# Optimization experiments

Hardware: AMD Instinct MI355X
Metric: run time of the kernel (lower is better)

## Reference

```python
import jax, jax.numpy as jnp
import numpy as np

HID = 1024
HEADS = 16
HEAD_DIM = HID // HEADS
MLP_HID = 4096
TEMB = 1024
EPS = 1e-6


def _ln(x):
    # LayerNorm without affine, eps=1e-6
    mu = jnp.mean(x, axis=-1, keepdims=True)
    var = jnp.var(x, axis=-1, keepdims=True)
    return (x - mu) * jax.lax.rsqrt(var + EPS)


def _modulate(x, shift, scale):
    return x * (1.0 + scale[:, None, :]) + shift[:, None, :]


def setup_inputs() -> dict:
    key = jax.random.key(0)
    ks = jax.random.split(key, 12)
    s = 0.02
    return {
        "x": jax.random.normal(ks[0], (8, 1024, HID), jnp.float32),
        "c": jax.random.normal(ks[1], (8, TEMB), jnp.float32),
        "W_qkv": jax.random.normal(ks[2], (HID, 3 * HID), jnp.float32) * s,
        "b_qkv": jnp.zeros((3 * HID,), jnp.float32),
        "W_proj": jax.random.normal(ks[3], (HID, HID), jnp.float32) * s,
        "b_proj": jnp.zeros((HID,), jnp.float32),
        "W_fc1": jax.random.normal(ks[4], (HID, MLP_HID), jnp.float32) * s,
        "b_fc1": jnp.zeros((MLP_HID,), jnp.float32),
        "W_fc2": jax.random.normal(ks[5], (MLP_HID, HID), jnp.float32) * s,
        "b_fc2": jnp.zeros((HID,), jnp.float32),
        "W_ada": jax.random.normal(ks[6], (TEMB, 6 * HID), jnp.float32) * s,
        "b_ada": jnp.zeros((6 * HID,), jnp.float32),
    }


def _attn(x, W_qkv, b_qkv, W_proj, b_proj):
    B, N, C = x.shape
    qkv = x @ W_qkv + b_qkv                      # [B,N,3C]
    qkv = qkv.reshape(B, N, 3, HEADS, HEAD_DIM)
    q, k, v = qkv[:, :, 0], qkv[:, :, 1], qkv[:, :, 2]  # [B,N,H,D]
    scale = HEAD_DIM ** -0.5
    logits = jnp.einsum('bnhd,bmhd->bhnm', q, k) * scale
    attn = jax.nn.softmax(logits, axis=-1)
    out = jnp.einsum('bhnm,bmhd->bnhd', attn, v).reshape(B, N, C)
    return out @ W_proj + b_proj


def reference(x, c, W_qkv, b_qkv, W_proj, b_proj, W_fc1, b_fc1, W_fc2, b_fc2, W_ada, b_ada):
    ada = jax.nn.silu(c) @ W_ada + b_ada          # [B,6C]
    shift_msa, scale_msa, gate_msa, shift_mlp, scale_mlp, gate_mlp = jnp.split(ada, 6, axis=1)

    h = _modulate(_ln(x), shift_msa, scale_msa)
    x = x + gate_msa[:, None, :] * _attn(h, W_qkv, b_qkv, W_proj, b_proj)

    h = _modulate(_ln(x), shift_mlp, scale_mlp)
    h = jax.nn.gelu(h @ W_fc1 + b_fc1, approximate=True) @ W_fc2 + b_fc2
    x = x + gate_mlp[:, None, :] * h
    return x
```

## Files before the change

### kernel.cpp

```cpp
#include <hip/hip_runtime.h>
#include <stdint.h>

typedef unsigned short u16;
typedef __attribute__((ext_vector_type(4))) float f32x4;
typedef __attribute__((ext_vector_type(8))) short bf16x8;
typedef bf16x8 bf16x8a __attribute__((may_alias));
typedef uint32_t u32a __attribute__((may_alias));

#define HID 1024
#define MLPD 4096
#define TEMB 1024
#define ADA_N 6144
#define SEQ 1024
#define BATCH 8
#define KCH 32
#define KCHLEN (TEMB / KCH)

__device__ __forceinline__ u16 f2bf_bits(float f) {
  uint32_t u = __float_as_uint(f);
  uint32_t r = (u + 0x7FFFu + ((u >> 16) & 1u)) >> 16;
  return (u16)r;
}

__device__ __forceinline__ uint32_t cvt_pk_bf16(float lo, float hi) {
  uint32_t r;
  asm("v_cvt_pk_bf16_f32 %0, %1, %2" : "=v"(r) : "v"(lo), "v"(hi));
  return r;
}

__device__ __forceinline__ float exp2_hw(float x) {
#if __has_builtin(__builtin_amdgcn_exp2f)
  return __builtin_amdgcn_exp2f(x);
#else
  return exp2f(x);
#endif
}

__device__ __forceinline__ void async_copy16(void* lds_dst, const void* g_src) {
  __builtin_amdgcn_global_load_lds(
      (const __attribute__((address_space(1))) void*)(uintptr_t)g_src,
      (__attribute__((address_space(3))) void*)(uint32_t)(uintptr_t)lds_dst,
      16, 0, 0);
}

__device__ __forceinline__ float gelu_tanh(float v) {
  float u = 0.7978845608028654f * (v + 0.044715f * v * v * v);
  float e = __expf(2.f * u);
  return v * e / (e + 1.f);
}

__global__ __launch_bounds__(256) void transpose_bf16(const float* __restrict__ W,
                                                      u16* __restrict__ Wt, int K, int N) {
  __shared__ float tile[32][33];
  int n0 = blockIdx.x * 32, k0 = blockIdx.y * 32;
  int tx = threadIdx.x & 31, ty = threadIdx.x >> 5;
#pragma unroll
  for (int i = 0; i < 4; i++)
    tile[ty + i * 8][tx] = W[(size_t)(k0 + ty + i * 8) * N + n0 + tx];
  __syncthreads();
#pragma unroll
  for (int i = 0; i < 4; i++)
    Wt[(size_t)(n0 + ty + i * 8) * K + k0 + tx] = f2bf_bits(tile[tx][ty + i * 8]);
}

__global__ __launch_bounds__(256) void ada_part(const float* __restrict__ c,
                                                const float* __restrict__ W,
                                                float* __restrict__ part) {
  __shared__ float sc[BATCH * KCHLEN];
  int t = threadIdx.x;
  int col = blockIdx.x * 256 + t;
  int kc = blockIdx.y;
  int k0 = kc * KCHLEN;
  for (int i = t; i < BATCH * KCHLEN; i += 256) {
    int b = i >> 5, kk = i & (KCHLEN - 1);
    float v = c[b * TEMB + k0 + kk];
    sc[i] = v / (1.f + __expf(-v));
  }
  __syncthreads();
  float acc[BATCH] = {};
  for (int kk = 0; kk < KCHLEN; kk++) {
    float w = W[(size_t)(k0 + kk) * ADA_N + col];
#pragma unroll
    for (int b = 0; b < BATCH; b++) acc[b] += sc[b * KCHLEN + kk] * w;
  }
#pragma unroll
  for (int b = 0; b < BATCH; b++)
    part[((size_t)kc * BATCH + b) * ADA_N + col] = acc[b];
}

__global__ __launch_bounds__(256) void ada_reduce(const float* __restrict__ part,
                                                  const float* __restrict__ bias,
                                                  float* __restrict__ out) {
  int i = blockIdx.x * 256 + threadIdx.x;
  int col = i % ADA_N, b = i / ADA_N;
  float s = bias[col];
#pragma unroll
  for (int kc = 0; kc < KCH; kc++)
    s += part[((size_t)kc * BATCH + b) * ADA_N + col];
  out[(size_t)b * ADA_N + col] = s;
}

__global__ __launch_bounds__(256) void ln_mod(const float* __restrict__ x,
                                              const float* __restrict__ ada,
                                              int shift_off, int scale_off,
                                              u16* __restrict__ h) {
  int row = blockIdx.x;
  int bb = row >> 10;
  int t = threadIdx.x;
  const float4 v = ((const float4*)(x + (size_t)row * HID))[t];
  float s = v.x + v.y + v.z + v.w;
  float sq = v.x * v.x + v.y * v.y + v.z * v.z + v.w * v.w;
#pragma unroll
  for (int off = 32; off >= 1; off >>= 1) {
    s += __shfl_xor(s, off);
    sq += __shfl_xor(sq, off);
  }
  __shared__ float red[8];
  int wid = t >> 6;
  if ((t & 63) == 0) { red[wid] = s; red[4 + wid] = sq; }
  __syncthreads();
  s = red[0] + red[1] + red[2] + red[3];
  sq = red[4] + red[5] + red[6] + red[7];
  float mu = s * (1.0f / HID);
  float rs = rsqrtf(sq * (1.0f / HID) - mu * mu + 1e-6f);
  const float4 sc = ((const float4*)(ada + (size_t)bb * ADA_N + scale_off))[t];
  const float4 sh = ((const float4*)(ada + (size_t)bb * ADA_N + shift_off))[t];
  ushort4 o;
  o.x = f2bf_bits((v.x - mu) * rs * (1.f + sc.x) + sh.x);
  o.y = f2bf_bits((v.y - mu) * rs * (1.f + sc.y) + sh.y);
  o.z = f2bf_bits((v.z - mu) * rs * (1.f + sc.z) + sh.z);
  o.w = f2bf_bits((v.w - mu) * rs * (1.f + sc.w) + sh.w);
  ((ushort4*)(h + (size_t)row * HID))[t] = o;
}


template <int NLOAD>
__device__ __forceinline__ void stage_tile(u16* dst, const u16* gsrc, int K, int koff, int t) {
#pragma unroll
  for (int i = 0; i < NLOAD; ++i) {
    int slot = i * 512 + t;
    int row = slot >> 3, cp = slot & 7;
    const u16* src = gsrc + (size_t)row * K + koff + ((cp ^ (row & 7)) << 3);
    async_copy16(dst + slot * 8, src);
  }
}

#define LDSRD(buf, row, kk) \
  (*(const bf16x8a*)&(buf)[(row) * 64 + ((((kk) * 4 + l4) ^ ((row) & 7)) << 3)])

template <int EPI, int BN>
__global__ __launch_bounds__(512, 2) void gemm8(const u16* __restrict__ A,
                                                const u16* __restrict__ Bt,
                                                const float* __restrict__ bias,
                                                void* __restrict__ Cout,
                                                const float* __restrict__ resid,
                                                const float* __restrict__ gate,
                                                int N, int K) {
  constexpr int NR = BN / 64;
  constexpr int BLOADS = BN / 64;
  constexpr int TOT = 4 + BLOADS;
  __shared__ u16 As[2][256 * 64];
  __shared__ u16 Bs[2][BN * 64];

  int t = threadIdx.x;
  int lane = t & 63, wid = t >> 6;
  int l15 = lane & 15, l4 = lane >> 4;
  int wr = wid >> 2, wc = wid & 3;
  int lid = blockIdx.x;
  int xcd = lid & 7, win = lid >> 3;
  int m0 = (xcd * 4 + (win & 3)) * 256;
  int n0 = (win >> 2) * BN;

  const u16* Abase = A + (size_t)m0 * K;
  const u16* Bbase = Bt + (size_t)n0 * K;
  f32x4 acc[8][NR] = {};

  u16 *cA = As[0], *cB = Bs[0], *nA = As[1], *nB = Bs[1];
  int nt = K / 64;
  stage_tile<4>(cA, Abase, K, 0, t);
  stage_tile<BLOADS>(cB, Bbase, K, 0, t);
  stage_tile<4>(nA, Abase, K, 64, t);
  stage_tile<BLOADS>(nB, Bbase, K, 64, t);
  if constexpr (TOT == 8) asm volatile("s_waitcnt vmcnt(8)" ::: "memory");
  else                    asm volatile("s_waitcnt vmcnt(6)" ::: "memory");
  __builtin_amdgcn_s_barrier();
  __builtin_amdgcn_sched_barrier(0);

  for (int ts = 0; ts < nt; ++ts) {
    bf16x8 bf[NR][2];
#pragma unroll
    for (int p = 0; p < 4; ++p) {
      if (p == 0) {
#pragma unroll
        for (int ni = 0; ni < NR; ++ni)
#pragma unroll
          for (int kk = 0; kk < 2; ++kk)
            bf[ni][kk] = LDSRD(cB, wc * (16 * NR) + ni * 16 + l15, kk);
      }
      bf16x8 af[2][2];
#pragma unroll
      for (int i = 0; i < 2; ++i)
#pragma unroll
        for (int kk = 0; kk < 2; ++kk)
          af[i][kk] = LDSRD(cA, wr * 128 + (p * 2 + i) * 16 + l15, kk);
      asm volatile("s_waitcnt lgkmcnt(0)" ::: "memory");
      __builtin_amdgcn_sched_barrier(0);
      __builtin_amdgcn_s_setprio(1);
#pragma unroll
      for (int i = 0; i < 2; ++i)
#pragma unroll
        for (int ni = 0; ni < NR; ++ni) {
          acc[p * 2 + i][ni] = __builtin_amdgcn_mfma_f32_16x16x32_bf16(af[i][0], bf[ni][0], acc[p * 2 + i][ni], 0, 0, 0);
          acc[p * 2 + i][ni] = __builtin_amdgcn_mfma_f32_16x16x32_bf16(af[i][1], bf[ni][1], acc[p * 2 + i][ni], 0, 0, 0);
        }
      __builtin_amdgcn_s_setprio(0);
      __builtin_amdgcn_sched_barrier(0);
      __builtin_amdgcn_s_barrier();
      __builtin_amdgcn_sched_barrier(0);
    }
    if (ts + 2 < nt) {
      stage_tile<4>(cA, Abase, K, (ts + 2) * 64, t);
      stage_tile<BLOADS>(cB, Bbase, K, (ts + 2) * 64, t);
      if constexpr (TOT == 8) asm volatile("s_waitcnt vmcnt(8)" ::: "memory");
      else                    asm volatile("s_waitcnt vmcnt(6)" ::: "memory");
    } else if (ts + 1 < nt) {
      asm volatile("s_waitcnt vmcnt(0)" ::: "memory");
    }
    __builtin_amdgcn_s_barrier();
    __builtin_amdgcn_sched_barrier(0);
    u16* tp;
    tp = cA; cA = nA; nA = tp;
    tp = cB; cB = nB; nB = tp;
  }

  int brow = m0 + wr * 128, bcol = n0 + wc * (16 * NR);
  int bb = m0 >> 10;
#pragma unroll
  for (int ni = 0; ni < NR; ++ni) {
    int col = bcol + ni * 16 + l15;
    float bv = bias[col];
    float gv = (EPI == 2) ? gate[(size_t)bb * ADA_N + col] : 0.f;
#pragma unroll
    for (int mi = 0; mi < 8; ++mi) {
#pragma unroll
      for (int r = 0; r < 4; ++r) {
        int row = brow + mi * 16 + l4 * 4 + r;
        float v = acc[mi][ni][r] + bv;
        if (EPI == 0) {
          ((u16*)Cout)[(size_t)row * N + col] = f2bf_bits(v);
        } else if (EPI == 1) {
          ((u16*)Cout)[(size_t)row * N + col] = f2bf_bits(gelu_tanh(v));
        } else {
          ((float*)Cout)[(size_t)row * N + col] =
              resid[(size_t)row * N + col] + gv * v;
        }
      }
    }
  }
}

__global__ __launch_bounds__(256, 3) void attn_kernel(const u16* __restrict__ qkv,
                                                      u16* __restrict__ O) {
  const int KSTR = 72, VSTR = 72, PSTR = 72;
  __shared__ u16 Ks[64 * 72];
  __shared__ u16 Vt[64 * 72];
  __shared__ u16 Plds[4 * 16 * 72];
  int t = threadIdx.x, lane = t & 63, wid = t >> 6;
  int l15 = lane & 15, l4 = lane >> 4;
  int work = ((blockIdx.x & 7) << 7) + (blockIdx.x >> 3);
  int bh = work >> 3, qt8 = work & 7;
  int b = bh >> 4, h = bh & 15;
  int bRow = b * SEQ;
  int hOff = h * 64;
  int q0 = qt8 * 128 + wid * 32;

  bf16x8 qr[2][2];
#pragma unroll
  for (int qt = 0; qt < 2; qt++) {
    const u16* qbase = qkv + (size_t)(bRow + q0 + qt * 16 + l15) * 3072 + hOff;
    qr[qt][0] = *(const bf16x8a*)(qbase + l4 * 8);
    qr[qt][1] = *(const bf16x8a*)(qbase + 32 + l4 * 8);
  }

  const float csc = 0.125f * 1.4426950408889634f;
  float mrow[2] = {-1e30f, -1e30f};
  float lsum[2] = {0.f, 0.f};
  f32x4 o[2][4] = {};
  u16* pw = Plds + wid * 16 * PSTR;

  for (int cc = 0; cc < 16; cc++) {
    int kv0 = cc * 64;
    __syncthreads();
#pragma unroll
    for (int i = 0; i < 2; i++) {
      int idx = i * 256 + t;
      int row = idx >> 3, ch = idx & 7;
      bf16x8 kk = *(const bf16x8a*)(qkv + (size_t)(bRow + kv0 + row) * 3072 + 1024 + hOff + ch * 8);
      *(bf16x8a*)&Ks[row * KSTR + ch * 8] = kk;
    }
#pragma unroll
    for (int i = 0; i < 2; i++) {
      int idx = i * 256 + t;
      int kv = idx >> 3, dc = idx & 7;
      bf16x8 vv = *(const bf16x8a*)(qkv + (size_t)(bRow + kv0 + kv) * 3072 + 2048 + hOff + dc * 8);
#pragma unroll
      for (int j = 0; j < 8; j++) {
        int jj = (j + dc) & 7;
        Vt[(dc * 8 + jj) * VSTR + kv] = ((const u16*)&vv)[jj];
      }
    }
    __syncthreads();

    bf16x8 ak[4][2];
#pragma unroll
    for (int kt = 0; kt < 4; kt++) {
      ak[kt][0] = *(const bf16x8a*)&Ks[(kt * 16 + l15) * KSTR + l4 * 8];
      ak[kt][1] = *(const bf16x8a*)&Ks[(kt * 16 + l15) * KSTR + 32 + l4 * 8];
    }
    f32x4 st[2][4];
#pragma unroll
    for (int qt = 0; qt < 2; qt++)
#pragma unroll
      for (int kt = 0; kt < 4; kt++) {
        f32x4 z = {0.f, 0.f, 0.f, 0.f};
        z = __builtin_amdgcn_mfma_f32_16x16x32_bf16(ak[kt][0], qr[qt][0], z, 0, 0, 0);
        z = __builtin_amdgcn_mfma_f32_16x16x32_bf16(ak[kt][1], qr[qt][1], z, 0, 0, 0);
        st[qt][kt] = z;
      }
    bf16x8 av[4][2];
#pragma unroll
    for (int dt = 0; dt < 4; dt++) {
      av[dt][0] = *(const bf16x8a*)&Vt[(dt * 16 + l15) * VSTR + l4 * 8];
      av[dt][1] = *(const bf16x8a*)&Vt[(dt * 16 + l15) * VSTR + 32 + l4 * 8];
    }

#pragma unroll
    for (int qt = 0; qt < 2; qt++) {
      float mx = st[qt][0][0];
#pragma unroll
      for (int kt = 0; kt < 4; kt++)
#pragma unroll
        for (int r = 0; r < 4; r++) mx = fmaxf(mx, st[qt][kt][r]);
      mx = fmaxf(mx, __shfl_xor(mx, 16));
      mx = fmaxf(mx, __shfl_xor(mx, 32));
      float mn = fmaxf(mrow[qt], mx * csc);
      float al = exp2_hw(mrow[qt] - mn);
      mrow[qt] = mn;
      float rs = 0.f;
#pragma unroll
      for (int kt = 0; kt < 4; kt++)
#pragma unroll
        for (int r = 0; r < 4; r++) {
          float p = exp2_hw(__builtin_fmaf(st[qt][kt][r], csc, -mn));
          st[qt][kt][r] = p;
          rs += p;
        }
      rs += __shfl_xor(rs, 16);
      rs += __shfl_xor(rs, 32);
      lsum[qt] = lsum[qt] * al + rs;
#pragma unroll
      for (int dt = 0; dt < 4; dt++) o[qt][dt] *= al;
#pragma unroll
      for (int kt = 0; kt < 4; kt++) {
#pragma unroll
        for (int hh = 0; hh < 2; hh++) {
          uint32_t pk = cvt_pk_bf16(st[qt][kt][2 * hh], st[qt][kt][2 * hh + 1]);
          *(u32a*)&pw[l15 * PSTR + kt * 16 + l4 * 4 + 2 * hh] = pk;
        }
      }
      asm volatile("s_waitcnt lgkmcnt(0)" ::: "memory");
      __builtin_amdgcn_sched_barrier(0);
      bf16x8 bp0 = *(const bf16x8a*)&pw[l15 * PSTR + l4 * 8];
      bf16x8 bp1 = *(const bf16x8a*)&pw[l15 * PSTR + 32 + l4 * 8];
#pragma unroll
      for (int dt = 0; dt < 4; dt++) {
        o[qt][dt] = __builtin_amdgcn_mfma_f32_16x16x32_bf16(av[dt][0], bp0, o[qt][dt], 0, 0, 0);
        o[qt][dt] = __builtin_amdgcn_mfma_f32_16x16x32_bf16(av[dt][1], bp1, o[qt][dt], 0, 0, 0);
      }
      asm volatile("s_waitcnt lgkmcnt(0)" ::: "memory");
      __builtin_amdgcn_sched_barrier(0);
    }
  }
#pragma unroll
  for (int qt = 0; qt < 2; qt++) {
    float inv = 1.f / lsum[qt];
    u16* orow = O + (size_t)(bRow + q0 + qt * 16 + l15) * HID + hOff;
#pragma unroll
    for (int dt = 0; dt < 4; dt++) {
      uint2 w;
      w.x = cvt_pk_bf16(o[qt][dt][0] * inv, o[qt][dt][1] * inv);
      w.y = cvt_pk_bf16(o[qt][dt][2] * inv, o[qt][dt][3] * inv);
      *(uint2*)(orow + dt * 16 + l4 * 4) = w;
    }
  }
}

extern "C" void kernel_launch(void* const* d_in, const int* in_sizes, int n_in,
                              void* d_out, int out_size, void* d_ws, size_t ws_size,
                              hipStream_t stream) {
  const float* x      = (const float*)d_in[0];
  const float* c      = (const float*)d_in[1];
  const float* W_qkv  = (const float*)d_in[2];
  const float* b_qkv  = (const float*)d_in[3];
  const float* W_proj = (const float*)d_in[4];
  const float* b_proj = (const float*)d_in[5];
  const float* W_fc1  = (const float*)d_in[6];
  const float* b_fc1  = (const float*)d_in[7];
  const float* W_fc2  = (const float*)d_in[8];
  const float* b_fc2  = (const float*)d_in[9];
  const float* W_ada  = (const float*)d_in[10];
  const float* b_ada  = (const float*)d_in[11];
  float* out = (float*)d_out;
  char* ws = (char*)d_ws;

  float* ada  = (float*)(ws + 0);
  u16* WtQKV  = (u16*)(ws + 196608);
  u16* WtP    = (u16*)(ws + 6488064);
  u16* WtF1   = (u16*)(ws + 8585216);
  u16* WtF2   = (u16*)(ws + 16973824);
  u16* hbuf   = (u16*)(ws + 25362432);
  u16* big    = (u16*)(ws + 42139648);
  float* apart = (float*)(ws + 42139648);

  transpose_bf16<<<dim3(3072 / 32, 1024 / 32), 256, 0, stream>>>(W_qkv, WtQKV, 1024, 3072);
  transpose_bf16<<<dim3(1024 / 32, 1024 / 32), 256, 0, stream>>>(W_proj, WtP, 1024, 1024);
  transpose_bf16<<<dim3(4096 / 32, 1024 / 32), 256, 0, stream>>>(W_fc1, WtF1, 1024, 4096);
  transpose_bf16<<<dim3(1024 / 32, 4096 / 32), 256, 0, stream>>>(W_fc2, WtF2, 4096, 1024);
  ada_part<<<dim3(ADA_N / 256, KCH), 256, 0, stream>>>(c, W_ada, apart);
  ada_reduce<<<(BATCH * ADA_N) / 256, 256, 0, stream>>>(apart, b_ada, ada);
  ln_mod<<<8192, 256, 0, stream>>>(x, ada, 0, 1024, hbuf);
  gemm8<0, 128><<<768, 512, 0, stream>>>(hbuf, WtQKV, b_qkv, big, nullptr, nullptr, 3072, 1024);
  attn_kernel<<<1024, 256, 0, stream>>>(big, hbuf);
  gemm8<2, 128><<<256, 512, 0, stream>>>(hbuf, WtP, b_proj, out, x, ada + 2048, 1024, 1024);
  ln_mod<<<8192, 256, 0, stream>>>(out, ada, 3072, 4096, hbuf);
  gemm8<1, 256><<<512, 512, 0, stream>>>(hbuf, WtF1, b_fc1, big, nullptr, nullptr, 4096, 1024);
  gemm8<2, 128><<<256, 512, 0, stream>>>(big, WtF2, b_fc2, out, out, ada + 5120, 1024, 4096);
}
```

Before: 405.1 us.

## Restructure GEMM main loop, stage epilogue through LDS, fix BN at 128

The GEMM kernel is rewritten to load all A and B fragments for a k-tile up front, issue the next async global-to-LDS prefetch before the MFMA block, and use one barrier pair per tile instead of per-subphase barriers. The epilogue now writes bf16 results into LDS and then emits coalesced 16-byte row stores, adding the residual in fp32 for the gated outputs. The FC1 GEMM drops its 256-wide tile for 128 with twice the blocks. The residual-epilogue path now rounds gate*v to bf16 before adding, which costs some precision, and holding more fragments in registers raises register pressure.

```diff
diff --git a/kernel.cpp b/kernel.cpp
--- a/kernel.cpp
+++ b/kernel.cpp
@@ -20,6 +20,10 @@
   uint32_t u = __float_as_uint(f);
   uint32_t r = (u + 0x7FFFu + ((u >> 16) & 1u)) >> 16;
   return (u16)r;
+}
+
+__device__ __forceinline__ float bf2f(u16 b) {
+  return __uint_as_float(((uint32_t)b) << 16);
 }
 
 __device__ __forceinline__ uint32_t cvt_pk_bf16(float lo, float hi) {
@@ -148,7 +152,7 @@
 #define LDSRD(buf, row, kk) \
   (*(const bf16x8a*)&(buf)[(row) * 64 + ((((kk) * 4 + l4) ^ ((row) & 7)) << 3)])
 
-template <int EPI, int BN>
+template <int EPI>
 __global__ __launch_bounds__(512, 2) void gemm8(const u16* __restrict__ A,
                                                 const u16* __restrict__ Bt,
                                                 const float* __restrict__ bias,
@@ -156,11 +160,11 @@
                                                 const float* __restrict__ resid,
                                                 const float* __restrict__ gate,
                                                 int N, int K) {
-  constexpr int NR = BN / 64;
-  constexpr int BLOADS = BN / 64;
-  constexpr int TOT = 4 + BLOADS;
-  __shared__ u16 As[2][256 * 64];
-  __shared__ u16 Bs[2][BN * 64];
+  __shared__ u16 lds[49152];
+  u16* const As0 = lds;
+  u16* const As1 = lds + 16384;
+  u16* const Bs0 = lds + 32768;
+  u16* const Bs1 = lds + 40960;
 
   int t = threadIdx.x;
   int lane = t & 63, wid = t >> 6;
@@ -169,91 +173,90 @@
   int lid = blockIdx.x;
   int xcd = lid & 7, win = lid >> 3;
   int m0 = (xcd * 4 + (win & 3)) * 256;
-  int n0 = (win >> 2) * BN;
+  int n0 = (win >> 2) * 128;
 
   const u16* Abase = A + (size_t)m0 * K;
   const u16* Bbase = Bt + (size_t)n0 * K;
-  f32x4 acc[8][NR] = {};
-
-  u16 *cA = As[0], *cB = Bs[0], *nA = As[1], *nB = Bs[1];
+  f32x4 acc[8][2] = {};
+
+  stage_tile<4>(As0, Abase, K, 0, t);
+  stage_tile<2>(Bs0, Bbase, K, 0, t);
+  stage_tile<4>(As1, Abase, K, 64, t);
+  stage_tile<2>(Bs1, Bbase, K, 64, t);
   int nt = K / 64;
-  stage_tile<4>(cA, Abase, K, 0, t);
-  stage_tile<BLOADS>(cB, Bbase, K, 0, t);
-  stage_tile<4>(nA, Abase, K, 64, t);
-  stage_tile<BLOADS>(nB, Bbase, K, 64, t);
-  if constexpr (TOT == 8) asm volatile("s_waitcnt vmcnt(8)" ::: "memory");
-  else                    asm volatile("s_waitcnt vmcnt(6)" ::: "memory");
-  __builtin_amdgcn_s_barrier();
-  __builtin_amdgcn_sched_barrier(0);
-
   for (int ts = 0; ts < nt; ++ts) {
-    bf16x8 bf[NR][2];
-#pragma unroll
-    for (int p = 0; p < 4; ++p) {
-      if (p == 0) {
-#pragma unroll
-        for (int ni = 0; ni < NR; ++ni)
-#pragma unroll
-          for (int kk = 0; kk < 2; ++kk)
-            bf[ni][kk] = LDSRD(cB, wc * (16 * NR) + ni * 16 + l15, kk);
-      }
-      bf16x8 af[2][2];
-#pragma unroll
-      for (int i = 0; i < 2; ++i)
-#pragma unroll
-        for (int kk = 0; kk < 2; ++kk)
-          af[i][kk] = LDSRD(cA, wr * 128 + (p * 2 + i) * 16 + l15, kk);
-      asm volatile("s_waitcnt lgkmcnt(0)" ::: "memory");
-      __builtin_amdgcn_sched_barrier(0);
-      __builtin_amdgcn_s_setprio(1);
-#pragma unroll
-      for (int i = 0; i < 2; ++i)
-#pragma unroll
-        for (int ni = 0; ni < NR; ++ni) {
-          acc[p * 2 + i][ni] = __builtin_amdgcn_mfma_f32_16x16x32_bf16(af[i][0], bf[ni][0], acc[p * 2 + i][ni], 0, 0, 0);
-          acc[p * 2 + i][ni] = __builtin_amdgcn_mfma_f32_16x16x32_bf16(af[i][1], bf[ni][1], acc[p * 2 + i][ni], 0, 0, 0);
-        }
-      __builtin_amdgcn_s_setprio(0);
-      __builtin_amdgcn_sched_barrier(0);
-      __builtin_amdgcn_s_barrier();
-      __builtin_amdgcn_sched_barrier(0);
-    }
+    u16* cA = (ts & 1) ? As1 : As0;
+    u16* cB = (ts & 1) ? Bs1 : Bs0;
+    if (ts == nt - 1) asm volatile("s_waitcnt vmcnt(0)" ::: "memory");
+    else              asm volatile("s_waitcnt vmcnt(6)" ::: "memory");
+    __builtin_amdgcn_s_barrier();
+    asm volatile("" ::: "memory");
+    bf16x8 bf[2][2], af[8][2];
+#pragma unroll
+    for (int ni = 0; ni < 2; ++ni)
+#pragma unroll
+      for (int kk = 0; kk < 2; ++kk)
+        bf[ni][kk] = LDSRD(cB, wc * 32 + ni * 16 + l15, kk);
+#pragma unroll
+    for (int mi = 0; mi < 8; ++mi)
+#pragma unroll
+      for (int kk = 0; kk < 2; ++kk)
+        af[mi][kk] = LDSRD(cA, wr * 128 + mi * 16 + l15, kk);
+    asm volatile("s_waitcnt lgkmcnt(0)" ::: "memory");
+    __builtin_amdgcn_s_barrier();
     if (ts + 2 < nt) {
       stage_tile<4>(cA, Abase, K, (ts + 2) * 64, t);
-      stage_tile<BLOADS>(cB, Bbase, K, (ts + 2) * 64, t);
-      if constexpr (TOT == 8) asm volatile("s_waitcnt vmcnt(8)" ::: "memory");
-      else                    asm volatile("s_waitcnt vmcnt(6)" ::: "memory");
-    } else if (ts + 1 < nt) {
-      asm volatile("s_waitcnt vmcnt(0)" ::: "memory");
-    }
-    __builtin_amdgcn_s_barrier();
-    __builtin_amdgcn_sched_barrier(0);
-    u16* tp;
-    tp = cA; cA = nA; nA = tp;
-    tp = cB; cB = nB; nB = tp;
-  }
-
-  int brow = m0 + wr * 128, bcol = n0 + wc * (16 * NR);
+      stage_tile<2>(cB, Bbase, K, (ts + 2) * 64, t);
+    }
+    __builtin_amdgcn_s_setprio(1);
+#pragma unroll
+    for (int mi = 0; mi < 8; ++mi)
+#pragma unroll
+      for (int ni = 0; ni < 2; ++ni) {
+        acc[mi][ni] = __builtin_amdgcn_mfma_f32_16x16x32_bf16(af[mi][0], bf[ni][0], acc[mi][ni], 0, 0, 0);
+        acc[mi][ni] = __builtin_amdgcn_mfma_f32_16x16x32_bf16(af[mi][1], bf[ni][1], acc[mi][ni], 0, 0, 0);
+      }
+    __builtin_amdgcn_s_setprio(0);
+  }
+
+  const int EST = 132;
   int bb = m0 >> 10;
 #pragma unroll
-  for (int ni = 0; ni < NR; ++ni) {
-    int col = bcol + ni * 16 + l15;
-    float bv = bias[col];
-    float gv = (EPI == 2) ? gate[(size_t)bb * ADA_N + col] : 0.f;
-#pragma unroll
-    for (int mi = 0; mi < 8; ++mi) {
+  for (int ni = 0; ni < 2; ++ni) {
+    int col = wc * 32 + ni * 16 + l15;
+    float bv = bias[n0 + col];
+    float gv = (EPI == 2) ? gate[(size_t)bb * ADA_N + n0 + col] : 0.f;
+#pragma unroll
+    for (int mi = 0; mi < 8; ++mi)
 #pragma unroll
       for (int r = 0; r < 4; ++r) {
-        int row = brow + mi * 16 + l4 * 4 + r;
+        int row = wr * 128 + mi * 16 + l4 * 4 + r;
         float v = acc[mi][ni][r] + bv;
-        if (EPI == 0) {
-          ((u16*)Cout)[(size_t)row * N + col] = f2bf_bits(v);
-        } else if (EPI == 1) {
-          ((u16*)Cout)[(size_t)row * N + col] = f2bf_bits(gelu_tanh(v));
-        } else {
-          ((float*)Cout)[(size_t)row * N + col] =
-              resid[(size_t)row * N + col] + gv * v;
-        }
+        if (EPI == 1) v = gelu_tanh(v);
+        if (EPI == 2) v = gv * v;
+        lds[row * EST + col] = f2bf_bits(v);
+      }
+  }
+  asm volatile("s_waitcnt lgkmcnt(0)" ::: "memory");
+  __builtin_amdgcn_s_barrier();
+  asm volatile("" ::: "memory");
+  {
+    int row = t >> 1, half = t & 1;
+    size_t grow = (size_t)(m0 + row) * N + n0 + half * 64;
+#pragma unroll
+    for (int j = 0; j < 8; ++j) {
+      bf16x8 v = *(const bf16x8a*)&lds[row * EST + half * 64 + j * 8];
+      if (EPI == 2) {
+        const float4* rp = (const float4*)&resid[grow + j * 8];
+        float4 o0 = rp[0], o1 = rp[1];
+        o0.x += bf2f((u16)v[0]); o0.y += bf2f((u16)v[1]);
+        o0.z += bf2f((u16)v[2]); o0.w += bf2f((u16)v[3]);
+        o1.x += bf2f((u16)v[4]); o1.y += bf2f((u16)v[5]);
+        o1.z += bf2f((u16)v[6]); o1.w += bf2f((u16)v[7]);
+        float4* op = (float4*)((float*)Cout + grow + j * 8);
+        op[0] = o0; op[1] = o1;
+      } else {
+        *(bf16x8a*)((u16*)Cout + grow + j * 8) = v;
       }
     }
   }
@@ -429,10 +432,10 @@
   ada_part<<<dim3(ADA_N / 256, KCH), 256, 0, stream>>>(c, W_ada, apart);
   ada_reduce<<<(BATCH * ADA_N) / 256, 256, 0, stream>>>(apart, b_ada, ada);
   ln_mod<<<8192, 256, 0, stream>>>(x, ada, 0, 1024, hbuf);
-  gemm8<0, 128><<<768, 512, 0, stream>>>(hbuf, WtQKV, b_qkv, big, nullptr, nullptr, 3072, 1024);
+  gemm8<0><<<768, 512, 0, stream>>>(hbuf, WtQKV, b_qkv, big, nullptr, nullptr, 3072, 1024);
   attn_kernel<<<1024, 256, 0, stream>>>(big, hbuf);
-  gemm8<2, 128><<<256, 512, 0, stream>>>(hbuf, WtP, b_proj, out, x, ada + 2048, 1024, 1024);
+  gemm8<2><<<256, 512, 0, stream>>>(hbuf, WtP, b_proj, out, x, ada + 2048, 1024, 1024);
   ln_mod<<<8192, 256, 0, stream>>>(out, ada, 3072, 4096, hbuf);
-  gemm8<1, 256><<<512, 512, 0, stream>>>(hbuf, WtF1, b_fc1, big, nullptr, nullptr, 4096, 1024);
-  gemm8<2, 128><<<256, 512, 0, stream>>>(big, WtF2, b_fc2, out, out, ada + 5120, 1024, 4096);
-}
+  gemm8<1><<<1024, 512, 0, stream>>>(hbuf, WtF1, b_fc1, big, nullptr, nullptr, 4096, 1024);
+  gemm8<2><<<256, 512, 0, stream>>>(big, WtF2, b_fc2, out, out, ada + 5120, 1024, 4096);
+}
```

Result: slower. 453.9 us (+12.1%).
